# Kernel tuning notes

Measured on AMD Instinct MI355X. Metric: run time of the kernel, lower is better.

The kernel has to match this reference:

```python
import jax, jax.numpy as jnp
import numpy as np

H = 8            # num_heads
DK = 256         # head_qk_dim
DV = 512         # head_v_dim
EPS = 1e-5
ROPE_BASE = 10000.0


def _rope(x):
    # x: [B, T, H, DK]; GPT-NeoX style (non-interleaved halves), seqlen_offset=0
    B, T, h, d = x.shape
    inv_freq = 1.0 / (ROPE_BASE ** (jnp.arange(0, d, 2, dtype=jnp.float32) / d))  # [d/2]
    t = jnp.arange(T, dtype=jnp.float32)
    freqs = t[:, None] * inv_freq[None, :]              # [T, d/2]
    cos = jnp.cos(freqs)[None, :, None, :]              # [1, T, 1, d/2]
    sin = jnp.sin(freqs)[None, :, None, :]
    x1, x2 = x[..., : d // 2], x[..., d // 2 :]
    return jnp.concatenate([x1 * cos - x2 * sin, x2 * cos + x1 * sin], axis=-1)


def setup_inputs() -> dict:
    key = jax.random.key(0)
    ks = jax.random.split(key, 7)
    hidden = 2048
    B, T = 2, 2048
    w = 0.02
    return {
        "hidden_states": jax.random.normal(ks[0], (B, T, hidden), jnp.float32),
        "Wq": jax.random.normal(ks[1], (hidden, H * DK), jnp.float32) * w,
        "Wk": jax.random.normal(ks[2], (hidden, H * DK), jnp.float32) * w,
        "Wv": jax.random.normal(ks[3], (hidden, H * DV), jnp.float32) * w,
        "Wg": jax.random.normal(ks[4], (hidden, H * DV), jnp.float32) * w,
        "Wo": jax.random.normal(ks[5], (H * DV, hidden), jnp.float32) * w,
        "g_norm_weight": jnp.ones((DV,), jnp.float32),
    }


def reference(hidden_states, Wq, Wk, Wv, Wg, Wo, g_norm_weight):
    B, T, _ = hidden_states.shape
    q = (hidden_states @ Wq).reshape(B, T, H, DK)
    k = (hidden_states @ Wk).reshape(B, T, H, DK)
    v = (hidden_states @ Wv).reshape(B, T, H, DV)
    g = (hidden_states @ Wg).reshape(B, T, H, DV)

    q = _rope(q)
    k = _rope(k)

    # per-head RetNet decay: gamma_h = 1 - 2^(-5-h)
    gamma = 1.0 - jnp.exp2(-5.0 - jnp.arange(H, dtype=jnp.float32))     # [H]
    idx = jnp.arange(T)
    diff = idx[:, None] - idx[None, :]                                   # [T, T]
    causal = diff >= 0
    log2g = jnp.log2(gamma)[:, None, None]                               # [H,1,1]
    D = jnp.where(causal[None], jnp.exp2(log2g * jnp.where(causal, diff, 0)[None]), 0.0)  # [H,T,T]

    scale = DK ** -0.5
    scores = jnp.einsum("bihd,bjhd->bhij", q * scale, k) * D[None]       # [B,H,T,T]
    o = jnp.einsum("bhij,bjhd->bihd", scores, v)                          # [B,T,H,DV]

    # fused RMSNorm (per head over DV) + swish gate
    rms = jax.lax.rsqrt(jnp.mean(o * o, axis=-1, keepdims=True) + EPS)
    o = o * rms * g_norm_weight
    o = o * (g * jax.nn.sigmoid(g))

    return o.reshape(B, T, H * DV) @ Wo
```

## Files before the change

kernel.cpp:

```cpp
#include <hip/hip_runtime.h>
#include <hip/hip_bf16.h>
#include <math.h>

#define NH 8
#define DKk 256
#define DVv 512
#define Bn 2
#define Tn 2048
#define HID 2048
#define EPSf 1e-5f

typedef __bf16 bf16x8 __attribute__((ext_vector_type(8)));
typedef float f32x4 __attribute__((ext_vector_type(4)));
typedef unsigned short us8 __attribute__((ext_vector_type(8)));
using bf16 = __hip_bfloat16;
typedef unsigned short ushort_t;

__device__ __forceinline__ void gload_lds16(const void* g, void* lds_base) {
  __builtin_amdgcn_global_load_lds(
      (const __attribute__((address_space(1))) void*)g,
      (__attribute__((address_space(3))) void*)lds_base, 16, 0, 0);
}

__device__ __forceinline__ ushort_t f2bf_raw(float f) {
  bf16 h = __float2bfloat16(f);
  return *reinterpret_cast<ushort_t*>(&h);
}
__device__ __forceinline__ float bf2f_raw(ushort_t u) {
  union { unsigned int i; float f; } v; v.i = ((unsigned int)u) << 16; return v.f;
}

__global__ void k_f32_to_bf16(const float4* __restrict__ in, ushort4* __restrict__ out, int n4) {
  int i = blockIdx.x * blockDim.x + threadIdx.x;
  if (i >= n4) return;
  float4 v = in[i];
  ushort4 o;
  o.x = f2bf_raw(v.x); o.y = f2bf_raw(v.y); o.z = f2bf_raw(v.z); o.w = f2bf_raw(v.w);
  out[i] = o;
}

__global__ void k_transpose_w(const float* __restrict__ W, bf16* __restrict__ WT, int K, int N) {
  __shared__ float t[32][33];
  int n0 = blockIdx.x * 32, k0 = blockIdx.y * 32;
  int tx = threadIdx.x, ty = threadIdx.y;
#pragma unroll
  for (int i = 0; i < 4; i++)
    t[ty + i * 8][tx] = W[(size_t)(k0 + ty + i * 8) * N + n0 + tx];
  __syncthreads();
#pragma unroll
  for (int i = 0; i < 4; i++)
    WT[(size_t)(n0 + ty + i * 8) * K + k0 + tx] = __float2bfloat16(t[tx][ty + i * 8]);
}

__global__ void k_build_vS(const ushort_t* __restrict__ v, ushort_t* __restrict__ vS) {
  __shared__ ushort_t t[32 * 520];
  const int tid = threadIdx.x;
  const int kt = blockIdx.x;
  const int bh = blockIdx.y;
  const int b = bh >> 3, h = bh & 7;
#pragma unroll
  for (int r = 0; r < 8; r++) {
    int j = r * 4 + (tid >> 6);
    int vec = tid & 63;
    us8 d = *(const us8*)(v + (((size_t)(b * Tn + kt * 32 + j) * NH + h) * DVv) + vec * 8);
    *(us8*)(&t[j * 520 + vec * 8]) = d;
  }
  __syncthreads();
#pragma unroll
  for (int u = 0; u < 8; u++) {
    int uid = u * 256 + tid;
    int chunk = uid >> 9;
    int dv = uid & 511;
    us8 o;
#pragma unroll
    for (int jj = 0; jj < 8; jj++) o[jj] = t[(chunk * 8 + jj) * 520 + dv];
    *(us8*)(vS + ((size_t)(bh * 64 + kt) * 2048 + chunk * 512 + dv) * 8) = o;
  }
}

__global__ void k_rope(bf16* __restrict__ x, float scale) {
  int tid = blockIdx.x * 256 + threadIdx.x;
  int i = tid & 127;
  int h = (tid >> 7) & 7;
  int t = (tid >> 10) & (Tn - 1);
  int b = tid >> 21;
  float inv = exp2f(-(float)i * (13.287712379549449f / 128.0f));
  float ang = (float)t * inv;
  float s, c;
  sincosf(ang, &s, &c);
  size_t base = ((size_t)(b * Tn + t) * NH + h) * DKk + i;
  float x1 = __bfloat162float(x[base]);
  float x2 = __bfloat162float(x[base + 128]);
  x[base]       = __float2bfloat16((x1 * c - x2 * s) * scale);
  x[base + 128] = __float2bfloat16((x2 * c + x1 * s) * scale);
}

template <bool OUT_BF16>
__global__ __launch_bounds__(256) void k_gemm(const bf16* __restrict__ A, const bf16* __restrict__ BT,
                                              void* __restrict__ Cout, int M, int N, int K) {
  __shared__ __align__(16) bf16 a_lds[128 * 32];
  __shared__ __align__(16) bf16 b_lds[128 * 32];
  const int tid = threadIdx.x;
  const int l = tid & 63;
  const int w = tid >> 6;
  const int wr = w >> 1, wc = w & 1;
  const int bid = blockIdx.y * gridDim.x + blockIdx.x;
  const int cpx = (gridDim.x * gridDim.y) >> 3;
  const int s = (bid & 7) * cpx + (bid >> 3);
  const int bx = s / gridDim.y, by = s % gridDim.y;
  const int m0 = by * 128, n0 = bx * 128;
  const int quad = l >> 4, c16 = l & 15;

  const int lrow = l >> 2;
  const int loff = (l & 3) * 16;
  const char* aG0 = (const char*)(A + (size_t)(m0 + w * 32 + lrow) * K) + loff;
  const char* aG1 = (const char*)(A + (size_t)(m0 + w * 32 + 16 + lrow) * K) + loff;
  const char* bG0 = (const char*)(BT + (size_t)(n0 + w * 32 + lrow) * K) + loff;
  const char* bG1 = (const char*)(BT + (size_t)(n0 + w * 32 + 16 + lrow) * K) + loff;
  char* aL0 = (char*)a_lds + w * 2048;
  char* aL1 = (char*)a_lds + w * 2048 + 1024;
  char* bL0 = (char*)b_lds + w * 2048;
  char* bL1 = (char*)b_lds + w * 2048 + 1024;

  f32x4 acc[4][4];
  const f32x4 fz = {0.f, 0.f, 0.f, 0.f};
#pragma unroll
  for (int r = 0; r < 4; r++)
#pragma unroll
    for (int c = 0; c < 4; c++) acc[r][c] = fz;

  for (int k0 = 0; k0 < K; k0 += 32) {
    __syncthreads();
    size_t kb = (size_t)k0 * 2;
    gload_lds16(aG0 + kb, aL0);
    gload_lds16(aG1 + kb, aL1);
    gload_lds16(bG0 + kb, bL0);
    gload_lds16(bG1 + kb, bL1);
    __syncthreads();
    bf16x8 af[4], bfv[4];
#pragma unroll
    for (int r = 0; r < 4; r++)
      af[r] = *(const bf16x8*)(a_lds + (wr * 64 + r * 16 + c16) * 32 + quad * 8);
#pragma unroll
    for (int c = 0; c < 4; c++)
      bfv[c] = *(const bf16x8*)(b_lds + (wc * 64 + c * 16 + c16) * 32 + quad * 8);
#pragma unroll
    for (int r = 0; r < 4; r++)
#pragma unroll
      for (int c = 0; c < 4; c++)
        acc[r][c] = __builtin_amdgcn_mfma_f32_16x16x32_bf16(af[r], bfv[c], acc[r][c], 0, 0, 0);
  }

#pragma unroll
  for (int r = 0; r < 4; r++)
#pragma unroll
    for (int c = 0; c < 4; c++)
#pragma unroll
      for (int rr = 0; rr < 4; rr++) {
        int m = m0 + wr * 64 + r * 16 + quad * 4 + rr;
        int n = n0 + wc * 64 + c * 16 + c16;
        float val = acc[r][c][rr];
        if (OUT_BF16) ((bf16*)Cout)[(size_t)m * N + n] = __float2bfloat16(val);
        else          ((float*)Cout)[(size_t)m * N + n] = val;
      }
}

#define BARX() asm volatile("s_barrier" ::: "memory")
#define LGKM0() { asm volatile("s_waitcnt lgkmcnt(0)" ::: "memory"); __builtin_amdgcn_sched_barrier(0); }
#define VMW8() asm volatile("s_waitcnt vmcnt(8)" ::: "memory")
#define VMW0() asm volatile("s_waitcnt vmcnt(0)" ::: "memory")
#define PRIO1 __builtin_amdgcn_s_setprio(1)
#define PRIO0 __builtin_amdgcn_s_setprio(0)

#define QUADX(MH, NHh)                                                             \
  { _Pragma("unroll") for (int kk_ = 0; kk_ < 2; ++kk_)                            \
    _Pragma("unroll") for (int mf_ = 0; mf_ < 4; ++mf_)                            \
    _Pragma("unroll") for (int nf_ = 0; nf_ < 2; ++nf_)                            \
      acc[(MH)*4 + mf_][(NHh)*2 + nf_] = __builtin_amdgcn_mfma_f32_16x16x32_bf16(  \
          ar[(MH)*4 + mf_][kk_], br[(NHh)*2 + nf_][kk_],                           \
          acc[(MH)*4 + mf_][(NHh)*2 + nf_], 0, 0, 0); }

__global__ __launch_bounds__(512, 2) void k_gemm8(const bf16* __restrict__ A, const bf16* __restrict__ BT,
                                                  bf16* __restrict__ O0, bf16* __restrict__ O1,
                                                  int nsplit, int M, int Ntot, int K) {
  extern __shared__ char lds[];
  const int tid = threadIdx.x;
  const int lane = tid & 63;
  const int w = tid >> 6;
  const int wr = w >> 2;
  const int wc = w & 3;
  const int quad = lane >> 4, c16 = lane & 15;
  const int bid = blockIdx.y * gridDim.x + blockIdx.x;
  const int cpx = (gridDim.x * gridDim.y) >> 3;
  const int sw = (bid & 7) * cpx + (bid >> 3);
  const int bx = sw / gridDim.y, by = sw % gridDim.y;
  const int m0 = by * 256, n0 = bx * 256;

  const int srow = (w << 4) | (lane >> 3);
  const int gsw = (((lane & 7) ^ (lane >> 3)) << 4);
  const size_t rowBytes = (size_t)K * 2;
  const char* aS = (const char*)(A + (size_t)(m0 + srow) * K) + gsw;
  const char* bS = (const char*)(BT + (size_t)(n0 + srow) * K) + gsw;

  auto stage = [&](int matB, int buf, int h, int t) {
    const char* base = (matB ? bS : aS) + (size_t)h * 128 * rowBytes + (size_t)t * 128;
    char* ldst = lds + buf * 65536 + matB * 32768 + h * 16384 + w * 2048;
    gload_lds16(base, ldst);
    gload_lds16(base + 8 * rowBytes, ldst + 1024);
  };
  auto ldA = [&](int buf, int mf, int kk) -> bf16x8 {
    int row = wr * 128 + mf * 16 + c16;
    return *(const bf16x8*)(lds + buf * 65536 + row * 128 + ((((kk << 2) | quad) ^ (c16 & 7)) << 4));
  };
  auto ldB = [&](int buf, int nf, int kk) -> bf16x8 {
    int row = wc * 64 + nf * 16 + c16;
    return *(const bf16x8*)(lds + buf * 65536 + 32768 + row * 128 + ((((kk << 2) | quad) ^ (c16 & 7)) << 4));
  };

  f32x4 acc[8][4];
  const f32x4 fz = {0.f, 0.f, 0.f, 0.f};
#pragma unroll
  for (int i = 0; i < 8; i++)
#pragma unroll
    for (int j = 0; j < 4; j++) acc[i][j] = fz;
  bf16x8 ar[8][2], br[4][2];

  const int nT = K >> 6;
  const int nIter = nT >> 1;

  stage(0, 0, 0, 0); stage(0, 0, 1, 0);
  stage(1, 0, 0, 0); stage(1, 0, 1, 0);
  stage(0, 1, 0, 1); stage(0, 1, 1, 1);
  stage(1, 1, 0, 1); stage(1, 1, 1, 1);
  VMW8();
  BARX();

  for (int it = 0; it < nIter; ++it) {
    const int t = it * 2;
    const bool last = (it == nIter - 1);
#pragma unroll
    for (int mf = 0; mf < 4; ++mf) { ar[mf][0] = ldA(0, mf, 0); ar[mf][1] = ldA(0, mf, 1); }
#pragma unroll
    for (int nf = 0; nf < 2; ++nf) { br[nf][0] = ldB(0, nf, 0); br[nf][1] = ldB(0, nf, 1); }
    BARX(); LGKM0();
    PRIO1; QUADX(0, 0); PRIO0;
    BARX();
#pragma unroll
    for (int mf = 4; mf < 8; ++mf) { ar[mf][0] = ldA(0, mf, 0); ar[mf][1] = ldA(0, mf, 1); }
#pragma unroll
    for (int nf = 2; nf < 4; ++nf) { br[nf][0] = ldB(0, nf, 0); br[nf][1] = ldB(0, nf, 1); }
    BARX(); LGKM0();
    PRIO1; QUADX(0, 1); PRIO0;
    BARX();
    if (!last) { stage(0, 0, 0, t + 2); stage(0, 0, 1, t + 2); }
    BARX();
    PRIO1; QUADX(1, 0); PRIO0;
    BARX();
    if (!last) { stage(1, 0, 0, t + 2); stage(1, 0, 1, t + 2); }
    BARX();
    PRIO1; QUADX(1, 1); PRIO0;
    if (!last) { VMW8(); } else { VMW0(); }
    BARX();
#pragma unroll
    for (int mf = 0; mf < 4; ++mf) { ar[mf][0] = ldA(1, mf, 0); ar[mf][1] = ldA(1, mf, 1); }
#pragma unroll
    for (int nf = 0; nf < 2; ++nf) { br[nf][0] = ldB(1, nf, 0); br[nf][1] = ldB(1, nf, 1); }
    BARX(); LGKM0();
    PRIO1; QUADX(0, 0); PRIO0;
    BARX();
#pragma unroll
    for (int mf = 4; mf < 8; ++mf) { ar[mf][0] = ldA(1, mf, 0); ar[mf][1] = ldA(1, mf, 1); }
#pragma unroll
    for (int nf = 2; nf < 4; ++nf) { br[nf][0] = ldB(1, nf, 0); br[nf][1] = ldB(1, nf, 1); }
    BARX(); LGKM0();
    PRIO1; QUADX(0, 1); PRIO0;
    BARX();
    if (!last) { stage(0, 1, 0, t + 3); stage(0, 1, 1, t + 3); }
    BARX();
    PRIO1; QUADX(1, 0); PRIO0;
    BARX();
    if (!last) { stage(1, 1, 0, t + 3); stage(1, 1, 1, t + 3); }
    BARX();
    PRIO1; QUADX(1, 1); PRIO0;
    if (!last) VMW8();
    BARX();
  }

  bf16* Ob; int ldo, nc0;
  if (n0 < nsplit) { Ob = O0; ldo = nsplit; nc0 = n0; }
  else             { Ob = O1; ldo = Ntot - nsplit; nc0 = n0 - nsplit; }
#pragma unroll
  for (int mf = 0; mf < 8; ++mf)
#pragma unroll
    for (int nf = 0; nf < 4; ++nf)
#pragma unroll
      for (int rr = 0; rr < 4; ++rr) {
        int m = m0 + wr * 128 + mf * 16 + quad * 4 + rr;
        int n = nc0 + wc * 64 + nf * 16 + c16;
        Ob[(size_t)m * ldo + n] = __float2bfloat16(acc[mf][nf][rr]);
      }
}

__global__ __launch_bounds__(256, 2) void k_retention(const bf16* __restrict__ q, const bf16* __restrict__ k,
                                                      const char* __restrict__ vS, const bf16* __restrict__ g,
                                                      const float* __restrict__ gnw, bf16* __restrict__ X) {
  __shared__ __align__(16) char smem[65536];
  ushort_t* p_lds = (ushort_t*)(smem + 32768);
  float* red = (float*)(smem + 38912);
  bf16* o_lds = (bf16*)smem;

  const int tid = threadIdx.x;
  const int l = tid & 63, w = tid >> 6;
  const int quad = l >> 4, c16 = l & 15;

  const int bid = blockIdx.x;
  const int xcd = bid & 7;
  const int slot = bid >> 3;
  const int bh = xcd + 8 * (slot & 1);
  const int b = bh >> 3, h = bh & 7;
  const int qt = 31 - (slot >> 1);
  const int q0 = qt * 64;

  bf16x8 qf[8];
  {
    const bf16* qrow = q + ((size_t)(b * Tn + q0 + w * 16 + c16) * NH + h) * DKk + quad * 8;
#pragma unroll
    for (int c = 0; c < 8; c++) qf[c] = *(const bf16x8*)(qrow + c * 32);
  }

  const float log2g = log2f(1.0f - exp2f(-5.0f - (float)h));

  f32x4 acc[4][8];
  const f32x4 fz = {0.f, 0.f, 0.f, 0.f};
#pragma unroll
  for (int rt = 0; rt < 4; rt++)
#pragma unroll
    for (int n = 0; n < 8; n++) acc[rt][n] = fz;

  const int ktmax = 2 * qt + 1;
  const float Dcut = 30.0f / (-log2g);
  int kt0 = (int)fmaxf(0.0f, floorf(((float)q0 - Dcut) * (1.0f / 32.0f)));

  const char* vS_tilebase = vS + (size_t)(bh * 64) * 32768;

  auto stageK = [&](int kt, int pbuf) {
#pragma unroll
    for (int i = 0; i < 4; i++) {
      int instr = w * 4 + i;
      int j = instr * 2 + (l >> 5);
      int chunk_g = (l & 31) ^ (j & 7);
      const char* gp = (const char*)(k + ((size_t)(b * Tn + kt * 32 + j) * NH + h) * DKk) + chunk_g * 16;
      gload_lds16(gp, smem + pbuf * 16384 + instr * 1024);
    }
  };

  stageK(kt0, 0);

  for (int kt = kt0; kt <= ktmax; kt++) {
    const int pb = (kt - kt0) & 1;
    __syncthreads();
    if (kt < ktmax) stageK(kt + 1, pb ^ 1);

    f32x4 sacc[2] = {fz, fz};
#pragma unroll
    for (int jt = 0; jt < 2; jt++)
#pragma unroll
      for (int c = 0; c < 8; c++) {
        const char* kp = smem + pb * 16384 + (jt * 16 + c16) * 512 + (((c * 4 + quad) ^ (c16 & 7)) * 16);
        bf16x8 bfrag = *(const bf16x8*)kp;
        sacc[jt] = __builtin_amdgcn_mfma_f32_16x16x32_bf16(qf[c], bfrag, sacc[jt], 0, 0, 0);
      }

#pragma unroll
    for (int jt = 0; jt < 2; jt++)
#pragma unroll
      for (int r = 0; r < 4; r++) {
        int ig = q0 + w * 16 + quad * 4 + r;
        int jg = kt * 32 + jt * 16 + c16;
        int d = ig - jg;
        float val = (d >= 0) ? sacc[jt][r] * exp2f(log2g * (float)d) : 0.0f;
        p_lds[(w * 16 + quad * 4 + r) * 40 + jt * 16 + c16] = f2bf_raw(val);
      }
    asm volatile("s_waitcnt lgkmcnt(0)" ::: "memory");
    __builtin_amdgcn_sched_barrier(0);
    __builtin_amdgcn_s_barrier();

    bf16x8 pa[4];
#pragma unroll
    for (int rt = 0; rt < 4; rt++)
      pa[rt] = *(const bf16x8*)((const char*)p_lds + (rt * 16 + c16) * 80 + quad * 16);
    const char* vt = vS_tilebase + (size_t)kt * 32768 + quad * 8192 + w * 2048 + c16 * 16;
#pragma unroll
    for (int n = 0; n < 8; n++) {
      bf16x8 bv = *(const bf16x8*)(vt + n * 256);
#pragma unroll
      for (int rt = 0; rt < 4; rt++)
        acc[rt][n] = __builtin_amdgcn_mfma_f32_16x16x32_bf16(pa[rt], bv, acc[rt][n], 0, 0, 0);
    }
  }

  __syncthreads();
#pragma unroll
  for (int rt = 0; rt < 4; rt++)
#pragma unroll
    for (int r = 0; r < 4; r++) {
      float s = 0.f;
#pragma unroll
      for (int n = 0; n < 8; n++) { float v = acc[rt][n][r]; s += v * v; }
      s += __shfl_xor(s, 1);
      s += __shfl_xor(s, 2);
      s += __shfl_xor(s, 4);
      s += __shfl_xor(s, 8);
      if (c16 == 0) red[(rt * 16 + quad * 4 + r) * 4 + w] = s;
    }
  __syncthreads();
  float ss[4][4];
#pragma unroll
  for (int rt = 0; rt < 4; rt++)
#pragma unroll
    for (int r = 0; r < 4; r++) {
      int row = rt * 16 + quad * 4 + r;
      float tot = red[row * 4] + red[row * 4 + 1] + red[row * 4 + 2] + red[row * 4 + 3];
      ss[rt][r] = rsqrtf(tot * (1.0f / DVv) + EPSf);
    }
  __syncthreads();

#pragma unroll
  for (int n = 0; n < 8; n++) {
    int col = w * 128 + n * 16 + c16;
    float gw = gnw[col];
#pragma unroll
    for (int rt = 0; rt < 4; rt++)
#pragma unroll
      for (int r = 0; r < 4; r++) {
        int row = rt * 16 + quad * 4 + r;
        o_lds[row * 512 + col] = __float2bfloat16(acc[rt][n][r] * ss[rt][r] * gw);
      }
  }
  __syncthreads();

#pragma unroll
  for (int it = 0; it < 16; it++) {
    int cid = it * 256 + tid;
    int row = cid >> 6;
    int cp = (cid & 63) * 8;
    const ushort_t* gp = (const ushort_t*)g + ((size_t)(b * Tn + q0 + row) * NH + h) * DVv + cp;
    us8 gv = *(const us8*)gp;
    us8 ov;
#pragma unroll
    for (int e = 0; e < 8; e++) {
      float gf = bf2f_raw(gv[e]);
      float gate = gf / (1.0f + expf(-gf));
      float of = __bfloat162float(o_lds[row * 512 + cp + e]);
      ov[e] = f2bf_raw(of * gate);
    }
    *(us8*)((ushort_t*)X + ((size_t)(b * Tn + q0 + row) * NH + h) * DVv + cp) = ov;
  }
}

extern "C" void kernel_launch(void* const* d_in, const int* in_sizes, int n_in,
                              void* d_out, int out_size, void* d_ws, size_t ws_size,
                              hipStream_t stream) {
  const float* hs  = (const float*)d_in[0];
  const float* Wq  = (const float*)d_in[1];
  const float* Wk  = (const float*)d_in[2];
  const float* Wv  = (const float*)d_in[3];
  const float* Wg  = (const float*)d_in[4];
  const float* Wo  = (const float*)d_in[5];
  const float* gnw = (const float*)d_in[6];
  float* out = (float*)d_out;
  char* ws = (char*)d_ws;

  bf16* hsb = (bf16*)(ws);
  bf16* WqT = (bf16*)(ws + 16777216);
  bf16* WkT = (bf16*)(ws + 25165824);
  bf16* WvT = (bf16*)(ws + 33554432);
  bf16* WgT = (bf16*)(ws + 50331648);
  char* vSb = ws;
  bf16* WoT = (bf16*)(ws + 33554432);
  bf16* qb = (bf16*)(ws + 67108864);
  bf16* kb = (bf16*)(ws + 83886080);
  bf16* vb = (bf16*)(ws + 100663296);
  bf16* gb = (bf16*)(ws + 134217728);
  bf16* Xb = vb;

  static bool attr_done = false;
  if (!attr_done) {
    hipFuncSetAttribute((const void*)k_gemm8, hipFuncAttributeMaxDynamicSharedMemorySize, 131072);
    attr_done = true;
  }

  dim3 tb(32, 8);

  k_f32_to_bf16<<<8192, 256, 0, stream>>>((const float4*)hs, (ushort4*)hsb, 2097152);
  k_transpose_w<<<dim3(HID / 32, HID / 32), tb, 0, stream>>>(Wq, WqT, HID, HID);
  k_transpose_w<<<dim3(HID / 32, HID / 32), tb, 0, stream>>>(Wk, WkT, HID, HID);
  k_transpose_w<<<dim3(NH * DVv / 32, HID / 32), tb, 0, stream>>>(Wv, WvT, HID, NH * DVv);
  k_transpose_w<<<dim3(NH * DVv / 32, HID / 32), tb, 0, stream>>>(Wg, WgT, HID, NH * DVv);
  k_gemm8<<<dim3(16, 16), 512, 131072, stream>>>(hsb, WqT, qb, kb, 2048, 4096, 4096, 2048);
  k_gemm8<<<dim3(32, 16), 512, 131072, stream>>>(hsb, WvT, vb, gb, 4096, 4096, 8192, 2048);
  k_rope<<<16384, 256, 0, stream>>>(qb, 0.0625f);
  k_rope<<<16384, 256, 0, stream>>>(kb, 1.0f);
  k_build_vS<<<dim3(64, 16), 256, 0, stream>>>((const ushort_t*)vb, (ushort_t*)vSb);
  k_transpose_w<<<dim3(HID / 32, NH * DVv / 32), tb, 0, stream>>>(Wo, WoT, NH * DVv, HID);
  k_retention<<<512, 256, 0, stream>>>(qb, kb, vSb, gb, gnw, Xb);
  k_gemm<false><<<dim3(16, 32), 256, 0, stream>>>(Xb, WoT, out, 4096, 2048, 4096);
}
```

Baseline: 695.2 us.

## Stage V tiles through LDS with double-buffered async loads in retention kernel

The retention kernel now copies each V tile into LDS alongside the K tile using asynchronous global-to-LDS loads, double-buffered so the next tile loads while the current one is computed. It uses partial vmcnt waits and explicit barriers in place of a single syncthreads. LDS use grows to about 102 KB, so launch bounds drop to one block per CU, and the block-to-(batch, head, q-tile) mapping changes. This removes direct global reads of V inside the MFMA loop at the cost of lower occupancy and lost XCD-aware placement.

```diff
diff --git a/kernel.cpp b/kernel.cpp
--- a/kernel.cpp
+++ b/kernel.cpp
@@ -301,12 +301,12 @@
       }
 }
 
-__global__ __launch_bounds__(256, 2) void k_retention(const bf16* __restrict__ q, const bf16* __restrict__ k,
+__global__ __launch_bounds__(256, 1) void k_retention(const bf16* __restrict__ q, const bf16* __restrict__ k,
                                                       const char* __restrict__ vS, const bf16* __restrict__ g,
                                                       const float* __restrict__ gnw, bf16* __restrict__ X) {
-  __shared__ __align__(16) char smem[65536];
-  ushort_t* p_lds = (ushort_t*)(smem + 32768);
-  float* red = (float*)(smem + 38912);
+  extern __shared__ char smem[];
+  ushort_t* p_lds = (ushort_t*)(smem + 98304);
+  float* red = (float*)(smem + 103424);
   bf16* o_lds = (bf16*)smem;
 
   const int tid = threadIdx.x;
@@ -314,11 +314,9 @@
   const int quad = l >> 4, c16 = l & 15;
 
   const int bid = blockIdx.x;
-  const int xcd = bid & 7;
-  const int slot = bid >> 3;
-  const int bh = xcd + 8 * (slot & 1);
+  const int qt = 31 - (bid >> 4);
+  const int bh = bid & 15;
   const int b = bh >> 3, h = bh & 7;
-  const int qt = 31 - (slot >> 1);
   const int q0 = qt * 64;
 
   bf16x8 qf[8];
@@ -343,23 +341,35 @@
 
   const char* vS_tilebase = vS + (size_t)(bh * 64) * 32768;
 
-  auto stageK = [&](int kt, int pbuf) {
+  auto stageKV = [&](int kt, int pbuf) {
 #pragma unroll
     for (int i = 0; i < 4; i++) {
       int instr = w * 4 + i;
       int j = instr * 2 + (l >> 5);
-      int chunk_g = (l & 31) ^ (j & 7);
-      const char* gp = (const char*)(k + ((size_t)(b * Tn + kt * 32 + j) * NH + h) * DKk) + chunk_g * 16;
+      int cg = (l & 31) ^ (j & 7);
+      const char* gp = (const char*)(k + ((size_t)(b * Tn + kt * 32 + j) * NH + h) * DKk) + cg * 16;
       gload_lds16(gp, smem + pbuf * 16384 + instr * 1024);
     }
+#pragma unroll
+    for (int i = 0; i < 8; i++) {
+      int instr = w * 8 + i;
+      const char* gp = vS_tilebase + (size_t)kt * 32768 + instr * 1024 + l * 16;
+      gload_lds16(gp, smem + 32768 + pbuf * 32768 + instr * 1024);
+    }
   };
 
-  stageK(kt0, 0);
+  stageKV(kt0, 0);
 
   for (int kt = kt0; kt <= ktmax; kt++) {
     const int pb = (kt - kt0) & 1;
-    __syncthreads();
-    if (kt < ktmax) stageK(kt + 1, pb ^ 1);
+    if (kt < ktmax) {
+      stageKV(kt + 1, pb ^ 1);
+      asm volatile("s_waitcnt vmcnt(12)" ::: "memory");
+    } else {
+      asm volatile("s_waitcnt vmcnt(0)" ::: "memory");
+    }
+    __builtin_amdgcn_sched_barrier(0);
+    __builtin_amdgcn_s_barrier();
 
     f32x4 sacc[2] = {fz, fz};
 #pragma unroll
@@ -389,14 +399,17 @@
 #pragma unroll
     for (int rt = 0; rt < 4; rt++)
       pa[rt] = *(const bf16x8*)((const char*)p_lds + (rt * 16 + c16) * 80 + quad * 16);
-    const char* vt = vS_tilebase + (size_t)kt * 32768 + quad * 8192 + w * 2048 + c16 * 16;
+    const char* v_lds = smem + 32768 + pb * 32768;
 #pragma unroll
     for (int n = 0; n < 8; n++) {
-      bf16x8 bv = *(const bf16x8*)(vt + n * 256);
+      bf16x8 bv = *(const bf16x8*)(v_lds + quad * 8192 + (w * 128 + n * 16 + c16) * 16);
 #pragma unroll
       for (int rt = 0; rt < 4; rt++)
         acc[rt][n] = __builtin_amdgcn_mfma_f32_16x16x32_bf16(pa[rt], bv, acc[rt][n], 0, 0, 0);
     }
+    asm volatile("s_waitcnt lgkmcnt(0)" ::: "memory");
+    __builtin_amdgcn_sched_barrier(0);
+    __builtin_amdgcn_s_barrier();
   }
 
   __syncthreads();
@@ -487,6 +500,7 @@
   static bool attr_done = false;
   if (!attr_done) {
     hipFuncSetAttribute((const void*)k_gemm8, hipFuncAttributeMaxDynamicSharedMemorySize, 131072);
+    hipFuncSetAttribute((const void*)k_retention, hipFuncAttributeMaxDynamicSharedMemorySize, 104448);
     attr_done = true;
   }
 
@@ -503,6 +517,6 @@
   k_rope<<<16384, 256, 0, stream>>>(kb, 1.0f);
   k_build_vS<<<dim3(64, 16), 256, 0, stream>>>((const ushort_t*)vb, (ushort_t*)vSb);
   k_transpose_w<<<dim3(HID / 32, NH * DVv / 32), tb, 0, stream>>>(Wo, WoT, NH * DVv, HID);
-  k_retention<<<512, 256, 0, stream>>>(qb, kb, vSb, gb, gnw, Xb);
+  k_retention<<<512, 256, 104448, stream>>>(qb, kb, vSb, gb, gnw, Xb);
   k_gemm<false><<<dim3(16, 32), 256, 0, stream>>>(Xb, WoT, out, 4096, 2048, 4096);
 }
```

Measured after the change: 676.8 us. -2.6%, faster.
